# Kernel tuning notes

Measured on AMD Instinct MI355X. Metric: run time of the kernel, lower is better.

The kernel has to match this reference:

```python
import jax, jax.numpy as jnp
import numpy as np

N, E = 50000, 400000
HID, HT = 128, 128
HEADS, C = 4, 128  # TransformerConv heads=4, out_channels=hidden_X


def setup_inputs() -> dict:
    key = jax.random.key(0)
    ks = jax.random.split(key, 16)
    s = lambda k, shape, fan: jax.random.normal(k, shape, jnp.float32) / np.sqrt(fan)
    return {
        "edge_index": jax.random.randint(ks[0], (2, E), 0, N, dtype=jnp.int32),
        "h_X": jax.random.normal(ks[1], (N, HID), jnp.float32),
        "h_t": jax.random.normal(ks[2], (1, HT), jnp.float32),
        # TransformerConv params: lin_query/key/value: (HID -> HEADS*C), lin_skip: (HID -> C)
        "Wq": s(ks[3], (HID, HEADS * C), HID), "bq": jnp.zeros((HEADS * C,), jnp.float32),
        "Wk": s(ks[4], (HID, HEADS * C), HID), "bk": jnp.zeros((HEADS * C,), jnp.float32),
        "Wv": s(ks[5], (HID, HEADS * C), HID), "bv": jnp.zeros((HEADS * C,), jnp.float32),
        "Wskip": s(ks[6], (HID, C), HID), "bskip": jnp.zeros((C,), jnp.float32),
        # update_X: Linear(HID+HT -> HID), LayerNorm(HID)
        "Wup": s(ks[7], (HID + HT, HID), HID + HT), "bup": jnp.zeros((HID,), jnp.float32),
        "gamma": jnp.ones((HID,), jnp.float32), "beta": jnp.zeros((HID,), jnp.float32),
    }


def transformer_conv(h_X, edge_index, Wq, bq, Wk, bk, Wv, bv, Wskip, bskip):
    n = h_X.shape[0]
    src, dst = edge_index[0], edge_index[1]  # messages flow src -> dst
    q = (h_X @ Wq + bq).reshape(n, HEADS, C)
    k = (h_X @ Wk + bk).reshape(n, HEADS, C)
    v = (h_X @ Wv + bv).reshape(n, HEADS, C)
    # per-edge attention scores [E, H]
    score = jnp.einsum('ehc,ehc->eh', q[dst], k[src]) / np.sqrt(C)
    # segment softmax over incoming edges of each destination node
    m = jax.ops.segment_max(score, dst, num_segments=n)          # [N, H]
    ex = jnp.exp(score - m[dst])                                 # [E, H]
    denom = jax.ops.segment_sum(ex, dst, num_segments=n)        # [N, H]
    alpha = ex / denom[dst]                                      # [E, H]
    agg = jax.ops.segment_sum(alpha[..., None] * v[src], dst, num_segments=n)  # [N, H, C]
    out = agg.mean(axis=1)                                       # concat=False -> mean over heads
    return out + h_X @ Wskip + bskip                             # root_weight=True


def reference(edge_index, h_X, h_t, Wq, bq, Wk, bk, Wv, bv, Wskip, bskip,
              Wup, bup, gamma, beta):
    n = h_X.shape[0]
    h_att = transformer_conv(h_X, edge_index, Wq, bq, Wk, bk, Wv, bv, Wskip, bskip)
    h_t_exp = jnp.broadcast_to(h_t, (n, h_t.shape[1]))
    h = jnp.concatenate([h_att, h_t_exp], axis=1)
    h = jax.nn.relu(h @ Wup + bup)
    # LayerNorm (eps=1e-5); Dropout is identity in eval
    mu = h.mean(axis=-1, keepdims=True)
    var = ((h - mu) ** 2).mean(axis=-1, keepdims=True)
    return (h - mu) / jnp.sqrt(var + 1e-5) * gamma + beta
```

## Files before the change

kernel.cpp:

```cpp
#include <hip/hip_runtime.h>

typedef unsigned short u16;
typedef unsigned int   u32;

#define HID   128
#define HEADS 4
#define CH    128
#define HC    512
#define UT    32

typedef __bf16 bf16x8v __attribute__((ext_vector_type(8)));
typedef float  f32x4v  __attribute__((ext_vector_type(4)));
union FragU { uint4 u; bf16x8v b; };

static __device__ __forceinline__ float bf2f(u16 u) {
  union { u32 u; float f; } x;
  x.u = ((u32)u) << 16;
  return x.f;
}
static __device__ __forceinline__ u16 f2bf(float f) {
  union { float f; u32 u; } x;
  x.f = f;
  u32 r = x.u + 0x7fffu + ((x.u >> 16) & 1u);
  return (u16)(r >> 16);
}

static __device__ __forceinline__ void unpack8(uint4 raw, float* dst) {
  dst[0] = bf2f((u16)(raw.x & 0xffffu));
  dst[1] = bf2f((u16)(raw.x >> 16));
  dst[2] = bf2f((u16)(raw.y & 0xffffu));
  dst[3] = bf2f((u16)(raw.y >> 16));
  dst[4] = bf2f((u16)(raw.z & 0xffffu));
  dst[5] = bf2f((u16)(raw.z >> 16));
  dst[6] = bf2f((u16)(raw.w & 0xffffu));
  dst[7] = bf2f((u16)(raw.w >> 16));
}

__global__ void zero_kernel(int* p, int n) {
  int i = blockIdx.x * 256 + threadIdx.x;
  if (i < n) p[i] = 0;
}

__global__ void hist_kernel(const int* dst_idx, int* deg, int E) {
  int e = blockIdx.x * 256 + threadIdx.x;
  if (e < E) atomicAdd(&deg[dst_idx[e]], 1);
}

__global__ void blocksum_kernel(const int* deg, int* bsums, int n) {
  __shared__ int buf[256];
  int i = blockIdx.x * 256 + threadIdx.x;
  int v = 0;
  if (i < n) v = deg[i];
  buf[threadIdx.x] = v;
  __syncthreads();
  for (int off = 128; off > 0; off >>= 1) {
    if (threadIdx.x < off) buf[threadIdx.x] += buf[threadIdx.x + off];
    __syncthreads();
  }
  if (threadIdx.x == 0) bsums[blockIdx.x] = buf[0];
}

__global__ void scanb_kernel(const int* bsums, int* boffs, int nb) {
  __shared__ int buf[256];
  __shared__ int carry_s;
  int tid = threadIdx.x;
  if (tid == 0) carry_s = 0;
  __syncthreads();
  for (int base = 0; base < nb; base += 256) {
    int i = base + tid;
    int v = 0;
    if (i < nb) v = bsums[i];
    buf[tid] = v;
    __syncthreads();
    for (int off = 1; off < 256; off <<= 1) {
      int t = 0;
      if (tid >= off) t = buf[tid - off];
      __syncthreads();
      buf[tid] += t;
      __syncthreads();
    }
    int incl = buf[tid] + carry_s;
    if (i < nb) boffs[i] = incl - v;
    __syncthreads();
    if (tid == 255) carry_s = incl;
    __syncthreads();
  }
}

__global__ void scanfinal_kernel(const int* deg, const int* boffs,
                                 int* row_ptr, int* cursor, int n) {
  __shared__ int buf[256];
  int tid = threadIdx.x;
  int i = blockIdx.x * 256 + tid;
  int v = 0;
  if (i < n) v = deg[i];
  buf[tid] = v;
  __syncthreads();
  for (int off = 1; off < 256; off <<= 1) {
    int t = 0;
    if (tid >= off) t = buf[tid - off];
    __syncthreads();
    buf[tid] += t;
    __syncthreads();
  }
  int incl = buf[tid] + boffs[blockIdx.x];
  if (i < n) {
    row_ptr[i + 1] = incl;
    cursor[i] = incl - v;
  }
  if (i == 0) row_ptr[0] = 0;
}

__global__ void scatter_kernel(const int* src_idx, const int* dst_idx,
                               int* cursor, int* col, int E) {
  int e = blockIdx.x * 256 + threadIdx.x;
  if (e < E) {
    int pos = atomicAdd(&cursor[dst_idx[e]], 1);
    col[pos] = src_idx[e];
  }
}

__global__ void packH_kernel(const float* __restrict__ hX,
                             u16* __restrict__ hpack, int N, int total) {
  int i = blockIdx.x * 256 + threadIdx.x;
  if (i >= total) return;
  int j = i & 7;
  int lane = (i >> 3) & 63;
  int kc = (i >> 9) & 3;
  int ntile = i >> 11;
  int node = ntile * 16 + (lane & 15);
  int k = kc * 32 + (lane >> 4) * 8 + j;
  float v = (node < N) ? hX[(size_t)node * HID + k] : 0.f;
  hpack[i] = f2bf(v);
}

__global__ void packW4_kernel(const float* __restrict__ Wq,
                              const float* __restrict__ Wk,
                              const float* __restrict__ Wv,
                              const float* __restrict__ Wsk,
                              u16* __restrict__ Wp, int total) {
  int i = blockIdx.x * 256 + threadIdx.x;
  if (i >= total) return;
  int j = i & 7;
  int lane = (i >> 3) & 63;
  int kc = (i >> 9) & 3;
  int ct = i >> 11;
  int n = ct * 16 + (lane & 15);
  int k = kc * 32 + (lane >> 4) * 8 + j;
  float w;
  if (n < 512) w = Wq[(size_t)k * HC + n];
  else if (n < 1024) w = Wk[(size_t)k * HC + (n - 512)];
  else if (n < 1536) w = Wv[(size_t)k * HC + (n - 1024)];
  else w = Wsk[(size_t)k * HID + (n - 1536)];
  Wp[i] = f2bf(w);
}

__global__ __launch_bounds__(256) void mfma_proj_kernel(
    const u16* __restrict__ hpack, const u16* __restrict__ Wp,
    const float* __restrict__ bq, const float* __restrict__ bk,
    const float* __restrict__ bv, const float* __restrict__ bsk,
    u16* __restrict__ qb, u16* __restrict__ kbuf, u16* __restrict__ vbuf,
    float* __restrict__ skipf, int N) {
  int t = threadIdx.x;
  int wv = t >> 6;
  int L = t & 63;
  int ct = blockIdx.y * 4 + wv;
  int nt0 = blockIdx.x * 4;

  f32x4v acc[4];
  for (int mt = 0; mt < 4; ++mt) acc[mt] = (f32x4v){0.f, 0.f, 0.f, 0.f};

  const u16* wb = Wp + (size_t)ct * 2048;
  const u16* hb = hpack + (size_t)nt0 * 2048;

  for (int kc = 0; kc < 4; ++kc) {
    FragU bf;
    bf.u = *(const uint4*)(wb + kc * 512 + L * 8);
    for (int mt = 0; mt < 4; ++mt) {
      FragU af;
      af.u = *(const uint4*)(hb + mt * 2048 + kc * 512 + L * 8);
      acc[mt] =
          __builtin_amdgcn_mfma_f32_16x16x32_bf16(af.b, bf.b, acc[mt], 0, 0, 0);
    }
  }

  int colq = L & 15;
  int quad = L >> 4;
  int n = ct * 16 + colq;
  u16* outB;
  const float* bias;
  int nl;
  int isF32 = 0;
  if (n < 512) {
    outB = qb; bias = bq; nl = n;
  } else if (n < 1024) {
    outB = kbuf; bias = bk; nl = n - 512;
  } else if (n < 1536) {
    outB = vbuf; bias = bv; nl = n - 1024;
  } else {
    outB = (u16*)skipf; bias = bsk; nl = n - 1536; isF32 = 1;
  }
  float bval = bias[nl];
  for (int mt = 0; mt < 4; ++mt) {
    for (int rg = 0; rg < 4; ++rg) {
      int node = (nt0 + mt) * 16 + quad * 4 + rg;
      if (node < N) {
        float val = acc[mt][rg] + bval;
        if (isF32) {
          skipf[(size_t)node * HID + nl] = val;
        } else {
          outB[(size_t)node * HC + nl] = f2bf(val);
        }
      }
    }
  }
}

__global__ void fused_attn_kernel(const u16* __restrict__ qb,
                                  const u16* __restrict__ kb,
                                  const u16* __restrict__ vb,
                                  const int* __restrict__ row_ptr,
                                  const int* __restrict__ col_src,
                                  float* out, int N) {
  int node = blockIdx.x * 4 + (threadIdx.x >> 6);
  if (node >= N) return;
  int lane = threadIdx.x & 63;
  int head = lane >> 4;
  int r = lane & 15;
  int foff = head * CH + r * 8;
  const float sscale = 0.08838834764831845f;

  float qf[8];
  unpack8(*(const uint4*)(qb + (size_t)node * HC + foff), qf);

  float m = -3.402823466e38f;
  float l = 0.f;
  float acc[8];
  for (int j = 0; j < 8; ++j) acc[j] = 0.f;

  int e0 = row_ptr[node];
  int e1 = row_ptr[node + 1];
  int e = e0;

  for (; e + 4 <= e1; e += 4) {
    int s0 = col_src[e];
    int s1 = col_src[e + 1];
    int s2 = col_src[e + 2];
    int s3 = col_src[e + 3];
    uint4 k0 = *(const uint4*)(kb + (size_t)s0 * HC + foff);
    uint4 k1 = *(const uint4*)(kb + (size_t)s1 * HC + foff);
    uint4 k2 = *(const uint4*)(kb + (size_t)s2 * HC + foff);
    uint4 k3 = *(const uint4*)(kb + (size_t)s3 * HC + foff);
    uint4 v0 = *(const uint4*)(vb + (size_t)s0 * HC + foff);
    uint4 v1 = *(const uint4*)(vb + (size_t)s1 * HC + foff);
    uint4 v2 = *(const uint4*)(vb + (size_t)s2 * HC + foff);
    uint4 v3 = *(const uint4*)(vb + (size_t)s3 * HC + foff);

    float kf0[8], kf1[8], kf2[8], kf3[8];
    unpack8(k0, kf0);
    unpack8(k1, kf1);
    unpack8(k2, kf2);
    unpack8(k3, kf3);
    float p0 = 0.f, p1 = 0.f, p2 = 0.f, p3 = 0.f;
    for (int j = 0; j < 8; ++j) {
      p0 = fmaf(kf0[j], qf[j], p0);
      p1 = fmaf(kf1[j], qf[j], p1);
      p2 = fmaf(kf2[j], qf[j], p2);
      p3 = fmaf(kf3[j], qf[j], p3);
    }
    p0 += __shfl_xor(p0, 1);
    p1 += __shfl_xor(p1, 1);
    p2 += __shfl_xor(p2, 1);
    p3 += __shfl_xor(p3, 1);
    p0 += __shfl_xor(p0, 2);
    p1 += __shfl_xor(p1, 2);
    p2 += __shfl_xor(p2, 2);
    p3 += __shfl_xor(p3, 2);
    p0 += __shfl_xor(p0, 4);
    p1 += __shfl_xor(p1, 4);
    p2 += __shfl_xor(p2, 4);
    p3 += __shfl_xor(p3, 4);
    p0 += __shfl_xor(p0, 8);
    p1 += __shfl_xor(p1, 8);
    p2 += __shfl_xor(p2, 8);
    p3 += __shfl_xor(p3, 8);
    float sc0 = p0 * sscale;
    float sc1 = p1 * sscale;
    float sc2 = p2 * sscale;
    float sc3 = p3 * sscale;
    float mnew = fmaxf(fmaxf(m, fmaxf(sc0, sc1)), fmaxf(sc2, sc3));
    float so = __expf(m - mnew);
    float pe0 = __expf(sc0 - mnew);
    float pe1 = __expf(sc1 - mnew);
    float pe2 = __expf(sc2 - mnew);
    float pe3 = __expf(sc3 - mnew);
    l = l * so + (pe0 + pe1) + (pe2 + pe3);
    float vf0[8], vf1[8], vf2[8], vf3[8];
    unpack8(v0, vf0);
    unpack8(v1, vf1);
    unpack8(v2, vf2);
    unpack8(v3, vf3);
    for (int j = 0; j < 8; ++j) {
      float add = fmaf(pe0, vf0[j],
                       fmaf(pe1, vf1[j], fmaf(pe2, vf2[j], pe3 * vf3[j])));
      acc[j] = fmaf(acc[j], so, add);
    }
    m = mnew;
  }

  for (; e < e1; ++e) {
    int s0 = col_src[e];
    uint4 k0 = *(const uint4*)(kb + (size_t)s0 * HC + foff);
    uint4 v0 = *(const uint4*)(vb + (size_t)s0 * HC + foff);
    float kf0[8];
    unpack8(k0, kf0);
    float p0 = 0.f;
    for (int j = 0; j < 8; ++j) p0 = fmaf(kf0[j], qf[j], p0);
    p0 += __shfl_xor(p0, 1);
    p0 += __shfl_xor(p0, 2);
    p0 += __shfl_xor(p0, 4);
    p0 += __shfl_xor(p0, 8);
    float sc0 = p0 * sscale;
    float mnew = fmaxf(m, sc0);
    float so = __expf(m - mnew);
    float pe0 = __expf(sc0 - mnew);
    l = l * so + pe0;
    float vf0[8];
    unpack8(v0, vf0);
    for (int j = 0; j < 8; ++j) acc[j] = fmaf(acc[j], so, pe0 * vf0[j]);
    m = mnew;
  }

  float inv = 0.f;
  if (l > 0.f) inv = 1.0f / l;
  float val[8];
  for (int j = 0; j < 8; ++j) {
    float x = acc[j] * inv;
    x += __shfl_xor(x, 16);
    x += __shfl_xor(x, 32);
    val[j] = x * 0.25f;
  }

  if (head == 0) {
    float* p = out + (size_t)node * HID + r * 8;
    float4 a = *(const float4*)(p);
    float4 b = *(const float4*)(p + 4);
    a.x += val[0]; a.y += val[1]; a.z += val[2]; a.w += val[3];
    b.x += val[4]; b.y += val[5]; b.z += val[6]; b.w += val[7];
    *(float4*)(p) = a;
    *(float4*)(p + 4) = b;
  }
}

__global__ void cvec_kernel(const float* h_t, const float* Wup,
                            const float* bup, float* cvec) {
  int c = threadIdx.x;
  float acc = bup[c];
  for (int k = 0; k < 128; ++k)
    acc = fmaf(h_t[k], Wup[(size_t)(128 + k) * 128 + c], acc);
  cvec[c] = acc;
}

__global__ __launch_bounds__(256) void ATTLayer_19396072308956_kernel(
    float* out, const float* __restrict__ Wup, const float* __restrict__ cvec,
    const float* __restrict__ gamma, const float* __restrict__ beta, int N) {
  __shared__ float Wl[64 * 128];
  __shared__ float Hl[UT * 128];
  int t = threadIdx.x;
  int n0 = blockIdx.x * UT;

  for (int i = t * 4; i < UT * 128; i += 1024) {
    int node = n0 + (i >> 7);
    float4 v;
    if (node < N) {
      v = *(const float4*)(out + (size_t)node * HID + (i & 127));
    } else {
      v.x = 0.f; v.y = 0.f; v.z = 0.f; v.w = 0.f;
    }
    *(float4*)(Hl + i) = v;
  }

  int wv = t >> 6;
  int r = t & 63;
  int c0 = 2 * r;
  float2 cv = *(const float2*)(cvec + c0);
  float a0[8];
  float a1[8];
  for (int j = 0; j < 8; ++j) {
    a0[j] = cv.x;
    a1[j] = cv.y;
  }

  for (int ph = 0; ph < 2; ++ph) {
    __syncthreads();
    for (int i = t * 4; i < 64 * 128; i += 1024) {
      *(float4*)(Wl + i) = *(const float4*)(Wup + (size_t)ph * 64 * 128 + i);
    }
    __syncthreads();
    const float* hbase = Hl + (wv * 8) * 128 + ph * 64;
#pragma unroll 8
    for (int k = 0; k < 64; ++k) {
      float2 w2 = *(const float2*)(Wl + k * 128 + c0);
      for (int j = 0; j < 8; ++j) {
        float h = hbase[j * 128 + k];
        a0[j] = fmaf(h, w2.x, a0[j]);
        a1[j] = fmaf(h, w2.y, a1[j]);
      }
    }
  }

  float2 g = *(const float2*)(gamma + c0);
  float2 b = *(const float2*)(beta + c0);
  for (int j = 0; j < 8; ++j) {
    int node = n0 + wv * 8 + j;
    float r0 = fmaxf(a0[j], 0.f);
    float r1 = fmaxf(a1[j], 0.f);
    float s = r0 + r1;
    for (int msk = 1; msk < 64; msk <<= 1) s += __shfl_xor(s, msk);
    float mean = s * (1.0f / 128.0f);
    float d0 = r0 - mean;
    float d1 = r1 - mean;
    float sq = d0 * d0 + d1 * d1;
    for (int msk = 1; msk < 64; msk <<= 1) sq += __shfl_xor(sq, msk);
    float rstd = rsqrtf(sq * (1.0f / 128.0f) + 1e-5f);
    if (node < N) {
      float2 o;
      o.x = d0 * rstd * g.x + b.x;
      o.y = d1 * rstd * g.y + b.y;
      *(float2*)(out + (size_t)node * HID + c0) = o;
    }
  }
}

extern "C" void kernel_launch(void* const* d_in, const int* in_sizes, int n_in,
                              void* d_out, int out_size, void* d_ws,
                              size_t ws_size, hipStream_t stream) {
  (void)n_in;
  (void)out_size;
  (void)ws_size;

  const int* edge_index = (const int*)d_in[0];
  const float* hX    = (const float*)d_in[1];
  const float* h_t   = (const float*)d_in[2];
  const float* Wq    = (const float*)d_in[3];
  const float* bq    = (const float*)d_in[4];
  const float* Wk    = (const float*)d_in[5];
  const float* bk    = (const float*)d_in[6];
  const float* Wv    = (const float*)d_in[7];
  const float* bv    = (const float*)d_in[8];
  const float* Wskip = (const float*)d_in[9];
  const float* bskip = (const float*)d_in[10];
  const float* Wup   = (const float*)d_in[11];
  const float* bup   = (const float*)d_in[12];
  const float* gamma = (const float*)d_in[13];
  const float* beta  = (const float*)d_in[14];

  const int E = in_sizes[0] / 2;
  const int N = in_sizes[1] / HID;
  const int* src_idx = edge_index;
  const int* dst_idx = edge_index + E;
  const int NB = (N + 255) / 256;
  const int NTILES = (N + 15) / 16;
  const int NTILES4 = ((NTILES + 3) / 4) * 4;

  char* w = (char*)d_ws;
  size_t off = 0;
  float* cvec = (float*)(w + off);
  off += 256 * 4;
  int* deg = (int*)(w + off);
  off += ((size_t)N * 4 + 255) / 256 * 256;
  int* row_ptr = (int*)(w + off);
  off += ((size_t)(N + 1) * 4 + 255) / 256 * 256;
  int* cursor = (int*)(w + off);
  off += ((size_t)N * 4 + 255) / 256 * 256;
  int* bsums = (int*)(w + off);
  off += ((size_t)NB * 4 + 255) / 256 * 256;
  int* boffs = (int*)(w + off);
  off += ((size_t)NB * 4 + 255) / 256 * 256;
  int* col = (int*)(w + off);
  off += ((size_t)E * 4 + 255) / 256 * 256;
  u16* hpack = (u16*)(w + off);
  off += ((size_t)NTILES4 * 2048 * 2 + 255) / 256 * 256;
  u16* Wp = (u16*)(w + off);
  off += ((size_t)128 * 1664 * 2 + 255) / 256 * 256;
  u16* bigA = (u16*)(w + off);
  off += ((size_t)N * HC * 2 + 255) / 256 * 256;
  u16* bigB = (u16*)(w + off);
  off += ((size_t)N * HC * 2 + 255) / 256 * 256;
  u16* bigC = (u16*)(w + off);
  off += ((size_t)N * HC * 2 + 255) / 256 * 256;

  float* out = (float*)d_out;

  zero_kernel<<<NB, 256, 0, stream>>>(deg, N);
  hist_kernel<<<(E + 255) / 256, 256, 0, stream>>>(dst_idx, deg, E);
  blocksum_kernel<<<NB, 256, 0, stream>>>(deg, bsums, N);
  scanb_kernel<<<1, 256, 0, stream>>>(bsums, boffs, NB);
  scanfinal_kernel<<<NB, 256, 0, stream>>>(deg, boffs, row_ptr, cursor, N);
  scatter_kernel<<<(E + 255) / 256, 256, 0, stream>>>(src_idx, dst_idx, cursor,
                                                      col, E);

  int totH = NTILES4 * 2048;
  packH_kernel<<<(totH + 255) / 256, 256, 0, stream>>>(hX, hpack, N, totH);
  packW4_kernel<<<(128 * 1664 + 255) / 256, 256, 0, stream>>>(
      Wq, Wk, Wv, Wskip, Wp, 128 * 1664);

  cvec_kernel<<<1, 128, 0, stream>>>(h_t, Wup, bup, cvec);

  mfma_proj_kernel<<<dim3(NTILES4 / 4, 26), 256, 0, stream>>>(
      hpack, Wp, bq, bk, bv, bskip, bigA, bigB, bigC, out, N);

  fused_attn_kernel<<<(N + 3) / 4, 256, 0, stream>>>(bigA, bigB, bigC, row_ptr,
                                                     col, out, N);

  ATTLayer_19396072308956_kernel<<<(N + UT - 1) / UT, 256, 0, stream>>>(
      out, Wup, cvec, gamma, beta, N);
}
```

Baseline: 432.5 us.

## Stage projection tiles in LDS with direct global-to-LDS loads and larger block tiles

The MFMA projection kernel now uses a 128-node by 128-column block tile. Both the packed activations and the packed weights are copied into shared memory with global_load_lds, so one staged load feeds several waves instead of each wave re-reading global memory. The grid swaps its axes so that the 13 column blocks vary fastest, and node padding goes to multiples of 8 tiles. The cvec kernel also splits its reduction across 512 threads. In exchange the kernel uses 64KB of LDS per block and 64 accumulator vectors per thread, which lowers occupancy.

```diff
diff --git a/kernel.cpp b/kernel.cpp
--- a/kernel.cpp
+++ b/kernel.cpp
@@ -34,6 +34,12 @@
   dst[5] = bf2f((u16)(raw.z >> 16));
   dst[6] = bf2f((u16)(raw.w & 0xffffu));
   dst[7] = bf2f((u16)(raw.w >> 16));
+}
+
+static __device__ __forceinline__ void gld_lds16(const u16* g, u16* l) {
+  __builtin_amdgcn_global_load_lds(
+      (__attribute__((address_space(1))) const void*)g,
+      (__attribute__((address_space(3))) void*)l, 16, 0, 0);
 }
 
 __global__ void zero_kernel(int* p, int n) {
@@ -161,55 +167,79 @@
     const float* __restrict__ bv, const float* __restrict__ bsk,
     u16* __restrict__ qb, u16* __restrict__ kbuf, u16* __restrict__ vbuf,
     float* __restrict__ skipf, int N) {
+  __shared__ u16 Al[8 * 2048];
+  __shared__ u16 Bl[8 * 2048];
   int t = threadIdx.x;
   int wv = t >> 6;
   int L = t & 63;
-  int ct = blockIdx.y * 4 + wv;
-  int nt0 = blockIdx.x * 4;
-
-  f32x4v acc[4];
-  for (int mt = 0; mt < 4; ++mt) acc[mt] = (f32x4v){0.f, 0.f, 0.f, 0.f};
-
-  const u16* wb = Wp + (size_t)ct * 2048;
-  const u16* hb = hpack + (size_t)nt0 * 2048;
-
+  int bx = blockIdx.x;
+  int my = blockIdx.y;
+
+  const u16* srcA = hpack + (size_t)my * (8 * 2048);
+  const u16* srcB = Wp + (size_t)bx * (8 * 2048);
+  int ldso = (t & 192) * 8;
+#pragma unroll
+  for (int it = 0; it < 8; ++it) {
+    gld_lds16(srcA + it * 2048 + t * 8, Al + it * 2048 + ldso);
+    gld_lds16(srcB + it * 2048 + t * 8, Bl + it * 2048 + ldso);
+  }
+  __syncthreads();
+
+  f32x4v acc[8][2];
+#pragma unroll
+  for (int mt = 0; mt < 8; ++mt) {
+    acc[mt][0] = (f32x4v){0.f, 0.f, 0.f, 0.f};
+    acc[mt][1] = (f32x4v){0.f, 0.f, 0.f, 0.f};
+  }
+
+#pragma unroll
   for (int kc = 0; kc < 4; ++kc) {
-    FragU bf;
-    bf.u = *(const uint4*)(wb + kc * 512 + L * 8);
-    for (int mt = 0; mt < 4; ++mt) {
-      FragU af;
-      af.u = *(const uint4*)(hb + mt * 2048 + kc * 512 + L * 8);
-      acc[mt] =
-          __builtin_amdgcn_mfma_f32_16x16x32_bf16(af.b, bf.b, acc[mt], 0, 0, 0);
+    FragU b0, b1;
+    b0.u = *(const uint4*)(Bl + (2 * wv) * 2048 + kc * 512 + L * 8);
+    b1.u = *(const uint4*)(Bl + (2 * wv + 1) * 2048 + kc * 512 + L * 8);
+#pragma unroll
+    for (int mt = 0; mt < 8; ++mt) {
+      FragU a;
+      a.u = *(const uint4*)(Al + mt * 2048 + kc * 512 + L * 8);
+      acc[mt][0] =
+          __builtin_amdgcn_mfma_f32_16x16x32_bf16(a.b, b0.b, acc[mt][0], 0, 0, 0);
+      acc[mt][1] =
+          __builtin_amdgcn_mfma_f32_16x16x32_bf16(a.b, b1.b, acc[mt][1], 0, 0, 0);
     }
   }
 
   int colq = L & 15;
   int quad = L >> 4;
-  int n = ct * 16 + colq;
-  u16* outB;
-  const float* bias;
-  int nl;
-  int isF32 = 0;
-  if (n < 512) {
-    outB = qb; bias = bq; nl = n;
-  } else if (n < 1024) {
-    outB = kbuf; bias = bk; nl = n - 512;
-  } else if (n < 1536) {
-    outB = vbuf; bias = bv; nl = n - 1024;
-  } else {
-    outB = (u16*)skipf; bias = bsk; nl = n - 1536; isF32 = 1;
-  }
-  float bval = bias[nl];
-  for (int mt = 0; mt < 4; ++mt) {
-    for (int rg = 0; rg < 4; ++rg) {
-      int node = (nt0 + mt) * 16 + quad * 4 + rg;
-      if (node < N) {
-        float val = acc[mt][rg] + bval;
-        if (isF32) {
-          skipf[(size_t)node * HID + nl] = val;
-        } else {
-          outB[(size_t)node * HC + nl] = f2bf(val);
+#pragma unroll
+  for (int cc = 0; cc < 2; ++cc) {
+    int ct = bx * 8 + 2 * wv + cc;
+    int n = ct * 16 + colq;
+    u16* outB;
+    const float* bias;
+    int nl;
+    int isF32 = 0;
+    if (n < 512) {
+      outB = qb; bias = bq; nl = n;
+    } else if (n < 1024) {
+      outB = kbuf; bias = bk; nl = n - 512;
+    } else if (n < 1536) {
+      outB = vbuf; bias = bv; nl = n - 1024;
+    } else {
+      outB = (u16*)skipf; bias = bsk; nl = n - 1536; isF32 = 1;
+    }
+    float bval = bias[nl];
+#pragma unroll
+    for (int mt = 0; mt < 8; ++mt) {
+#pragma unroll
+      for (int rg = 0; rg < 4; ++rg) {
+        int node = (my * 8 + mt) * 16 + quad * 4 + rg;
+        if (node < N) {
+          float val = acc[mt][cc][rg] + bval;
+          if (isF32) {
+            skipf[(size_t)node * HID + nl] = val;
+          } else {
+            outB[(size_t)node * HC + nl] = f2bf(val);
+          }
         }
       }
     }
@@ -354,11 +384,16 @@
 
 __global__ void cvec_kernel(const float* h_t, const float* Wup,
                             const float* bup, float* cvec) {
-  int c = threadIdx.x;
-  float acc = bup[c];
-  for (int k = 0; k < 128; ++k)
+  __shared__ float part[4][128];
+  int c = threadIdx.x & 127;
+  int kc = threadIdx.x >> 7;
+  float acc = 0.f;
+  for (int k = kc * 32; k < kc * 32 + 32; ++k)
     acc = fmaf(h_t[k], Wup[(size_t)(128 + k) * 128 + c], acc);
-  cvec[c] = acc;
+  part[kc][c] = acc;
+  __syncthreads();
+  if (kc == 0)
+    cvec[c] = part[0][c] + part[1][c] + part[2][c] + part[3][c] + bup[c];
 }
 
 __global__ __launch_bounds__(256) void ATTLayer_19396072308956_kernel(
@@ -461,7 +496,7 @@
   const int* dst_idx = edge_index + E;
   const int NB = (N + 255) / 256;
   const int NTILES = (N + 15) / 16;
-  const int NTILES4 = ((NTILES + 3) / 4) * 4;
+  const int NTILES8 = ((NTILES + 7) / 8) * 8;
 
   char* w = (char*)d_ws;
   size_t off = 0;
@@ -480,7 +515,7 @@
   int* col = (int*)(w + off);
   off += ((size_t)E * 4 + 255) / 256 * 256;
   u16* hpack = (u16*)(w + off);
-  off += ((size_t)NTILES4 * 2048 * 2 + 255) / 256 * 256;
+  off += ((size_t)NTILES8 * 2048 * 2 + 255) / 256 * 256;
   u16* Wp = (u16*)(w + off);
   off += ((size_t)128 * 1664 * 2 + 255) / 256 * 256;
   u16* bigA = (u16*)(w + off);
@@ -500,14 +535,14 @@
   scatter_kernel<<<(E + 255) / 256, 256, 0, stream>>>(src_idx, dst_idx, cursor,
                                                       col, E);
 
-  int totH = NTILES4 * 2048;
+  int totH = NTILES8 * 2048;
   packH_kernel<<<(totH + 255) / 256, 256, 0, stream>>>(hX, hpack, N, totH);
   packW4_kernel<<<(128 * 1664 + 255) / 256, 256, 0, stream>>>(
       Wq, Wk, Wv, Wskip, Wp, 128 * 1664);
 
-  cvec_kernel<<<1, 128, 0, stream>>>(h_t, Wup, bup, cvec);
-
-  mfma_proj_kernel<<<dim3(NTILES4 / 4, 26), 256, 0, stream>>>(
+  cvec_kernel<<<1, 512, 0, stream>>>(h_t, Wup, bup, cvec);
+
+  mfma_proj_kernel<<<dim3(13, NTILES8 / 8), 256, 0, stream>>>(
       hpack, Wp, bq, bk, bv, bskip, bigA, bigB, bigC, out, N);
 
   fused_attn_kernel<<<(N + 3) / 4, 256, 0, stream>>>(bigA, bigB, bigC, row_ptr,
```

New measurement: 456.9 us. 1.06x slower.
